# Kernel tuning notes

Measured on AMD Instinct MI355X. Metric: run time of the kernel, lower is better.

Reference implementation:

```python
import jax, jax.numpy as jnp
import numpy as np

N, E = 50000, 800000
IN_DIM, E_DIM, OUT_DIM, H = 128, 32, 16, 4
NEG_SLOPE = 0.2


def setup_inputs() -> dict:
    key = jax.random.key(0)
    ks = jax.random.split(key, 9)
    return {
        "feat": jax.random.normal(ks[0], (N, IN_DIM), jnp.float32),
        "edge_attr": jax.random.normal(ks[1], (E, E_DIM), jnp.float32),
        "src": jax.random.randint(ks[2], (E,), 0, N),
        "dst": jax.random.randint(ks[3], (E,), 0, N),
        "W_fc": jax.random.normal(ks[4], (OUT_DIM * H, IN_DIM), jnp.float32) * 0.1,
        "W_edge": jax.random.normal(ks[5], (OUT_DIM * H, E_DIM), jnp.float32) * 0.1,
        "attn_h": jax.random.normal(ks[6], (1, H, OUT_DIM), jnp.float32) * 0.1,
        "attn_t": jax.random.normal(ks[7], (1, H, OUT_DIM), jnp.float32) * 0.1,
        "attn_e": jax.random.normal(ks[8], (1, H, OUT_DIM), jnp.float32) * 0.1,
        "bias": jnp.zeros((1, H, OUT_DIM), jnp.float32),
    }


def reference(feat, edge_attr, src, dst, W_fc, W_edge, attn_h, attn_t, attn_e, bias):
    n = feat.shape[0]
    # node / edge projections
    feat_ = (feat @ W_fc.T).reshape(n, H, OUT_DIM)          # [N,H,D]
    eh = (feat_ * attn_h).sum(-1)                            # [N,H]
    et = (feat_ * attn_t).sum(-1)                            # [N,H]
    feat_e = (edge_attr @ W_edge.T).reshape(-1, H, OUT_DIM)  # [E,H,D]
    ee = (feat_e * attn_e).sum(-1)                           # [E,H]
    # per-edge attention logits: u_add_e then e_add_v, then leaky relu
    e = eh[src] + ee + et[dst]                               # [E,H]
    e = jnp.where(e > 0, e, NEG_SLOPE * e)
    # edge softmax grouped by destination node
    e_max = jax.ops.segment_max(e, dst, num_segments=n)      # [N,H]
    e_max = jnp.where(jnp.isfinite(e_max), e_max, 0.0)
    a = jnp.exp(e - e_max[dst])                              # [E,H]
    a_sum = jax.ops.segment_sum(a, dst, num_segments=n)      # [N,H]
    a = a / jnp.where(a_sum[dst] > 0, a_sum[dst], 1.0)
    # u_mul_e + sum aggregation
    msg = feat_[src] * a[:, :, None]                         # [E,H,D]
    rst = jax.ops.segment_sum(msg, dst, num_segments=n)      # [N,H,D]
    rst = rst + bias
    return rst.reshape(n, H * OUT_DIM)                       # concat_out
```

## Files before the change

kernel.cpp:

```cpp
#include <hip/hip_runtime.h>

#define NN 50000
#define EE 800000
#define IND 128
#define EDD 32
#define ODD 16
#define NH 4
#define HD 64
#define NEG_SLOPE 0.2f
#define NBLK ((NN + 255) / 256)

__global__ __launch_bounds__(256)
void k_init(int* __restrict__ deg) {
    int i = blockIdx.x * 256 + threadIdx.x;
    if (i < NN) deg[i] = 0;
}

__global__ __launch_bounds__(256)
void k_prep(const float* __restrict__ W_fc, const float* __restrict__ W_edge,
            const float* __restrict__ attn_e,
            float* __restrict__ Wt, float* __restrict__ w_ee) {
    int i = blockIdx.x * 256 + threadIdx.x;
    if (i < HD * IND) {
        int k = i >> 6, j = i & 63;
        Wt[i] = W_fc[j * IND + k];
    }
    if (i < NH * EDD) {
        int h = i >> 5, k = i & 31;
        float s = 0.f;
        for (int d = 0; d < ODD; ++d)
            s += W_edge[(h * ODD + d) * EDD + k] * attn_e[h * ODD + d];
        w_ee[i] = s;
    }
}

__global__ __launch_bounds__(256)
void k_node(const float* __restrict__ feat, const float* __restrict__ Wt,
            const float* __restrict__ attn_h, const float* __restrict__ attn_t,
            float* __restrict__ feat_ws, float2* __restrict__ eh2,
            float2* __restrict__ et2) {
    int n = blockIdx.x * 256 + threadIdx.x;
    int half = blockIdx.y;
    if (n >= NN) return;
    const int jbase = half * 32;
    float4 row[32];
    const float4* fr4 = (const float4*)(feat + (long)n * IND);
#pragma unroll
    for (int q = 0; q < 32; ++q) row[q] = fr4[q];
    float acc[32];
#pragma unroll
    for (int j = 0; j < 32; ++j) acc[j] = 0.f;
#pragma unroll 4
    for (int k0 = 0; k0 < 32; ++k0) {
        float f[4] = {row[k0].x, row[k0].y, row[k0].z, row[k0].w};
#pragma unroll
        for (int kk = 0; kk < 4; ++kk) {
            const float* w = Wt + (k0 * 4 + kk) * HD + jbase;
#pragma unroll
            for (int j = 0; j < 32; ++j) acc[j] += f[kk] * w[j];
        }
    }
    float4* d4 = (float4*)(feat_ws + (long)n * HD + jbase);
#pragma unroll
    for (int q = 0; q < 8; ++q)
        d4[q] = make_float4(acc[q*4], acc[q*4+1], acc[q*4+2], acc[q*4+3]);
    float sh[2], st[2];
#pragma unroll
    for (int hh = 0; hh < 2; ++hh) {
        sh[hh] = 0.f; st[hh] = 0.f;
        int hg = half * 2 + hh;
#pragma unroll
        for (int d = 0; d < ODD; ++d) {
            float av = acc[hh * ODD + d];
            sh[hh] += av * attn_h[hg * ODD + d];
            st[hh] += av * attn_t[hg * ODD + d];
        }
    }
    eh2[n * 2 + half] = make_float2(sh[0], sh[1]);
    et2[n * 2 + half] = make_float2(st[0], st[1]);
}

__global__ __launch_bounds__(256)
void k_hist(const int* __restrict__ dst, int* __restrict__ deg, int* __restrict__ rank) {
    int e = blockIdx.x * 256 + threadIdx.x;
    if (e < EE) rank[e] = atomicAdd(&deg[dst[e]], 1);
}

__global__ __launch_bounds__(256)
void k_scan1(const int* __restrict__ deg, int* __restrict__ offs, int* __restrict__ part) {
    __shared__ int s[256];
    int t = threadIdx.x, i = blockIdx.x * 256 + t;
    int v = (i < NN) ? deg[i] : 0;
    s[t] = v;
    __syncthreads();
#pragma unroll
    for (int o = 1; o < 256; o <<= 1) {
        int u = (t >= o) ? s[t - o] : 0;
        __syncthreads();
        if (t >= o) s[t] += u;
        __syncthreads();
    }
    if (i < NN) offs[i] = s[t] - v;
    if (t == 255) part[blockIdx.x] = s[255];
}

__global__ __launch_bounds__(256)
void k_scan2(int* __restrict__ part) {
    __shared__ int s[256];
    int t = threadIdx.x;
    int v = (t < NBLK) ? part[t] : 0;
    s[t] = v;
    __syncthreads();
#pragma unroll
    for (int o = 1; o < 256; o <<= 1) {
        int u = (t >= o) ? s[t - o] : 0;
        __syncthreads();
        if (t >= o) s[t] += u;
        __syncthreads();
    }
    if (t < NBLK) part[t] = s[t] - v;
}

__global__ __launch_bounds__(256)
void k_scan3(int* __restrict__ offs, const int* __restrict__ part) {
    int i = blockIdx.x * 256 + threadIdx.x;
    if (i < NN) offs[i] += part[i >> 8];
}

__global__ __launch_bounds__(256)
void k_logit(const float* __restrict__ edge_attr, const int* __restrict__ src,
             const int* __restrict__ dst, const float* __restrict__ w_ee,
             const float4* __restrict__ eh4, const float4* __restrict__ et4,
             const int* __restrict__ offs, const int* __restrict__ rank,
             float4* __restrict__ e_buf4, int* __restrict__ perm) {
    int e = blockIdx.x * 256 + threadIdx.x;
    if (e >= EE) return;
    int s_ = src[e], d_ = dst[e];
    int pos = offs[d_] + rank[e];
    float4 vh = eh4[s_];
    float4 vt = et4[d_];
    const float* ea = edge_attr + (long)e * EDD;
    float f[EDD];
#pragma unroll
    for (int c = 0; c < 8; ++c) {
        float4 p = *(const float4*)(ea + c * 4);
        f[c*4+0] = p.x; f[c*4+1] = p.y; f[c*4+2] = p.z; f[c*4+3] = p.w;
    }
    float x[NH];
#pragma unroll
    for (int h = 0; h < NH; ++h) {
        float s = 0.f;
#pragma unroll
        for (int k = 0; k < EDD; ++k) s += f[k] * w_ee[h * EDD + k];
        x[h] = s;
    }
    x[0] += vh.x + vt.x; x[1] += vh.y + vt.y;
    x[2] += vh.z + vt.z; x[3] += vh.w + vt.w;
#pragma unroll
    for (int h = 0; h < NH; ++h) {
        float v = x[h];
        v = v > 0.f ? v : NEG_SLOPE * v;
        x[h] = __expf(v);
    }
    e_buf4[e] = make_float4(x[0], x[1], x[2], x[3]);
    perm[pos] = e;
}

__global__ __launch_bounds__(256)
void k_reduce(const int* __restrict__ offs, const int* __restrict__ deg,
              const float* __restrict__ e_buf, const int* __restrict__ perm,
              const int* __restrict__ src, const float* __restrict__ feat_ws,
              const float* __restrict__ bias, float* __restrict__ out) {
    int wid = (blockIdx.x * 256 + threadIdx.x) >> 6;
    int lane = threadIdx.x & 63;
    if (wid >= NN) return;
    int start = __builtin_amdgcn_readfirstlane(offs[wid]);
    int dn    = __builtin_amdgcn_readfirstlane(deg[wid]);
    int h = lane >> 4;
    int q = lane & 15;
    float acc = 0.f, l = 0.f;

    for (int c0 = 0; c0 < dn; c0 += 16) {
        int rem = dn - c0; if (rem > 16) rem = 16;
        int qq = (q < rem) ? q : (rem - 1);
        int   e_q = perm[start + c0 + qq];
        int   s_q = src[e_q];
        float a_q = (q < rem) ? e_buf[(long)e_q * 4 + h] : 0.f;
        float f[16];
#pragma unroll
        for (int i = 0; i < 16; ++i) {
            int si = __shfl(s_q, i);
            f[i] = feat_ws[(long)si * HD + lane];
        }
#pragma unroll
        for (int i = 0; i < 16; ++i) {
            float ai = __shfl(a_q, (lane & 48) + i);
            l += ai;
            acc += ai * f[i];
        }
    }
    float res = (l > 0.f) ? acc / l : 0.f;
    out[(long)wid * HD + lane] = res + bias[lane];
}

extern "C" void kernel_launch(void* const* d_in, const int* in_sizes, int n_in,
                              void* d_out, int out_size, void* d_ws, size_t ws_size,
                              hipStream_t stream) {
    const float* feat      = (const float*)d_in[0];
    const float* edge_attr = (const float*)d_in[1];
    const int*   src       = (const int*)d_in[2];
    const int*   dst       = (const int*)d_in[3];
    const float* W_fc      = (const float*)d_in[4];
    const float* W_edge    = (const float*)d_in[5];
    const float* attn_h    = (const float*)d_in[6];
    const float* attn_t    = (const float*)d_in[7];
    const float* attn_e    = (const float*)d_in[8];
    const float* bias      = (const float*)d_in[9];
    float* out             = (float*)d_out;

    float* ws        = (float*)d_ws;
    float4* e_buf4   = (float4*)ws;
    float4* eh4      = e_buf4 + EE;
    float4* et4      = eh4 + NN;
    float*  feat_ws  = (float*)(et4 + NN);
    float*  Wt       = feat_ws + (long)NN * HD;
    float*  w_ee     = Wt + HD * IND;
    int*    perm     = (int*)(w_ee + NH * EDD);
    int*    rank     = perm + EE;
    int*    deg      = rank + EE;
    int*    offs     = deg + NN;
    int*    part     = offs + NN;

    k_init<<<NBLK, 256, 0, stream>>>(deg);
    k_prep<<<(HD * IND + 255) / 256, 256, 0, stream>>>(W_fc, W_edge, attn_e, Wt, w_ee);
    dim3 ngrid(NBLK, 2);
    k_node<<<ngrid, 256, 0, stream>>>(feat, Wt, attn_h, attn_t, feat_ws,
                                      (float2*)eh4, (float2*)et4);
    k_hist<<<(EE + 255) / 256, 256, 0, stream>>>(dst, deg, rank);
    k_scan1<<<NBLK, 256, 0, stream>>>(deg, offs, part);
    k_scan2<<<1, 256, 0, stream>>>(part);
    k_scan3<<<NBLK, 256, 0, stream>>>(offs, part);
    k_logit<<<(EE + 255) / 256, 256, 0, stream>>>(edge_attr, src, dst, w_ee, eh4, et4,
                                                  offs, rank, e_buf4, perm);
    k_reduce<<<(NN * 64 + 255) / 256, 256, 0, stream>>>(offs, deg, (const float*)e_buf4,
                                                        perm, src, feat_ws, bias, out);
}
```

Measured before the change: 350.1 us.

## Store node features as bf16 and write attention in dst-sorted order for reduce

Projected node features are packed to bf16, which halves the bytes gathered per edge in the reduce kernel. The logit kernel is split into a permutation scatter and an attention kernel that runs in sorted (dst) order, writing attention weights and source ids contiguously. The reduce kernel can then read them with coalesced loads instead of double indirection through perm. The init and prep kernels are fused and the node loop is fully unrolled. The cost is bf16 rounding error on the features, an extra launch, and random edge_attr reads in k_att.

```diff
diff --git a/kernel.cpp b/kernel.cpp
--- a/kernel.cpp
+++ b/kernel.cpp
@@ -10,17 +10,21 @@
 #define NEG_SLOPE 0.2f
 #define NBLK ((NN + 255) / 256)
 
-__global__ __launch_bounds__(256)
-void k_init(int* __restrict__ deg) {
+typedef unsigned int u32;
+typedef unsigned short u16;
+
+__device__ __forceinline__ float bf2f(u32 u) { return __uint_as_float(u << 16); }
+__device__ __forceinline__ u16 f2bf(float f) {
+    u32 b = __float_as_uint(f);
+    return (u16)((b + 0x7FFF + ((b >> 16) & 1)) >> 16);
+}
+
+__global__ __launch_bounds__(256)
+void k_init_prep(int* __restrict__ deg, const float* __restrict__ W_fc,
+                 const float* __restrict__ W_edge, const float* __restrict__ attn_e,
+                 float* __restrict__ Wt, float* __restrict__ w_ee) {
     int i = blockIdx.x * 256 + threadIdx.x;
     if (i < NN) deg[i] = 0;
-}
-
-__global__ __launch_bounds__(256)
-void k_prep(const float* __restrict__ W_fc, const float* __restrict__ W_edge,
-            const float* __restrict__ attn_e,
-            float* __restrict__ Wt, float* __restrict__ w_ee) {
-    int i = blockIdx.x * 256 + threadIdx.x;
     if (i < HD * IND) {
         int k = i >> 6, j = i & 63;
         Wt[i] = W_fc[j * IND + k];
@@ -37,7 +41,7 @@
 __global__ __launch_bounds__(256)
 void k_node(const float* __restrict__ feat, const float* __restrict__ Wt,
             const float* __restrict__ attn_h, const float* __restrict__ attn_t,
-            float* __restrict__ feat_ws, float2* __restrict__ eh2,
+            u16* __restrict__ feat_bf, float2* __restrict__ eh2,
             float2* __restrict__ et2) {
     int n = blockIdx.x * 256 + threadIdx.x;
     int half = blockIdx.y;
@@ -47,10 +51,11 @@
     const float4* fr4 = (const float4*)(feat + (long)n * IND);
 #pragma unroll
     for (int q = 0; q < 32; ++q) row[q] = fr4[q];
+    asm volatile("" ::: "memory");
     float acc[32];
 #pragma unroll
     for (int j = 0; j < 32; ++j) acc[j] = 0.f;
-#pragma unroll 4
+#pragma unroll
     for (int k0 = 0; k0 < 32; ++k0) {
         float f[4] = {row[k0].x, row[k0].y, row[k0].z, row[k0].w};
 #pragma unroll
@@ -60,10 +65,14 @@
             for (int j = 0; j < 32; ++j) acc[j] += f[kk] * w[j];
         }
     }
-    float4* d4 = (float4*)(feat_ws + (long)n * HD + jbase);
-#pragma unroll
-    for (int q = 0; q < 8; ++q)
-        d4[q] = make_float4(acc[q*4], acc[q*4+1], acc[q*4+2], acc[q*4+3]);
+    u32 pk[16];
+#pragma unroll
+    for (int q = 0; q < 16; ++q)
+        pk[q] = (u32)f2bf(acc[q * 2]) | ((u32)f2bf(acc[q * 2 + 1]) << 16);
+    uint4* d4 = (uint4*)((u32*)(feat_bf + (long)n * HD + jbase));
+#pragma unroll
+    for (int q = 0; q < 4; ++q)
+        d4[q] = make_uint4(pk[q*4], pk[q*4+1], pk[q*4+2], pk[q*4+3]);
     float sh[2], st[2];
 #pragma unroll
     for (int hh = 0; hh < 2; ++hh) {
@@ -128,24 +137,30 @@
 }
 
 __global__ __launch_bounds__(256)
-void k_logit(const float* __restrict__ edge_attr, const int* __restrict__ src,
-             const int* __restrict__ dst, const float* __restrict__ w_ee,
-             const float4* __restrict__ eh4, const float4* __restrict__ et4,
-             const int* __restrict__ offs, const int* __restrict__ rank,
-             float4* __restrict__ e_buf4, int* __restrict__ perm) {
+void k_perm(const int* __restrict__ dst, const int* __restrict__ rank,
+            const int* __restrict__ offs, int* __restrict__ perm) {
     int e = blockIdx.x * 256 + threadIdx.x;
-    if (e >= EE) return;
+    if (e < EE) perm[offs[dst[e]] + rank[e]] = e;
+}
+
+__global__ __launch_bounds__(256)
+void k_att(const float* __restrict__ edge_attr, const int* __restrict__ src,
+           const int* __restrict__ dst, const float* __restrict__ w_ee,
+           const float4* __restrict__ eh4, const float4* __restrict__ et4,
+           const int* __restrict__ perm, float4* __restrict__ a4,
+           int* __restrict__ ssrc) {
+    int pos = blockIdx.x * 256 + threadIdx.x;
+    if (pos >= EE) return;
+    int e = perm[pos];
     int s_ = src[e], d_ = dst[e];
-    int pos = offs[d_] + rank[e];
     float4 vh = eh4[s_];
     float4 vt = et4[d_];
-    const float* ea = edge_attr + (long)e * EDD;
-    float f[EDD];
-#pragma unroll
-    for (int c = 0; c < 8; ++c) {
-        float4 p = *(const float4*)(ea + c * 4);
-        f[c*4+0] = p.x; f[c*4+1] = p.y; f[c*4+2] = p.z; f[c*4+3] = p.w;
-    }
+    const float4* ea = (const float4*)(edge_attr + (long)e * EDD);
+    float4 r[8];
+#pragma unroll
+    for (int c = 0; c < 8; ++c) r[c] = ea[c];
+    asm volatile("" ::: "memory");
+    const float* f = (const float*)r;
     float x[NH];
 #pragma unroll
     for (int h = 0; h < NH; ++h) {
@@ -162,15 +177,15 @@
         v = v > 0.f ? v : NEG_SLOPE * v;
         x[h] = __expf(v);
     }
-    e_buf4[e] = make_float4(x[0], x[1], x[2], x[3]);
-    perm[pos] = e;
+    a4[pos] = make_float4(x[0], x[1], x[2], x[3]);
+    ssrc[pos] = s_;
 }
 
 __global__ __launch_bounds__(256)
 void k_reduce(const int* __restrict__ offs, const int* __restrict__ deg,
-              const float* __restrict__ e_buf, const int* __restrict__ perm,
-              const int* __restrict__ src, const float* __restrict__ feat_ws,
-              const float* __restrict__ bias, float* __restrict__ out) {
+              const float* __restrict__ a_flat, const int* __restrict__ ssrc,
+              const u16* __restrict__ feat_bf, const float* __restrict__ bias,
+              float* __restrict__ out) {
     int wid = (blockIdx.x * 256 + threadIdx.x) >> 6;
     int lane = threadIdx.x & 63;
     if (wid >= NN) return;
@@ -182,21 +197,22 @@
 
     for (int c0 = 0; c0 < dn; c0 += 16) {
         int rem = dn - c0; if (rem > 16) rem = 16;
+        float av = (lane < rem * 4) ? a_flat[(start + c0) * 4 + lane] : 0.f;
+        float a_q = __shfl(av, 4 * (lane & 15) + (lane >> 4));
+        if (q >= rem) a_q = 0.f;
         int qq = (q < rem) ? q : (rem - 1);
-        int   e_q = perm[start + c0 + qq];
-        int   s_q = src[e_q];
-        float a_q = (q < rem) ? e_buf[(long)e_q * 4 + h] : 0.f;
-        float f[16];
+        int s_q = ssrc[start + c0 + qq];
+        u32 uf[16];
 #pragma unroll
         for (int i = 0; i < 16; ++i) {
             int si = __shfl(s_q, i);
-            f[i] = feat_ws[(long)si * HD + lane];
+            uf[i] = feat_bf[(long)si * HD + lane];
         }
 #pragma unroll
         for (int i = 0; i < 16; ++i) {
             float ai = __shfl(a_q, (lane & 48) + i);
             l += ai;
-            acc += ai * f[i];
+            acc += ai * bf2f(uf[i]);
         }
     }
     float res = (l > 0.f) ? acc / l : 0.f;
@@ -218,30 +234,31 @@
     const float* bias      = (const float*)d_in[9];
     float* out             = (float*)d_out;
 
-    float* ws        = (float*)d_ws;
-    float4* e_buf4   = (float4*)ws;
-    float4* eh4      = e_buf4 + EE;
-    float4* et4      = eh4 + NN;
-    float*  feat_ws  = (float*)(et4 + NN);
-    float*  Wt       = feat_ws + (long)NN * HD;
-    float*  w_ee     = Wt + HD * IND;
-    int*    perm     = (int*)(w_ee + NH * EDD);
-    int*    rank     = perm + EE;
-    int*    deg      = rank + EE;
-    int*    offs     = deg + NN;
-    int*    part     = offs + NN;
-
-    k_init<<<NBLK, 256, 0, stream>>>(deg);
-    k_prep<<<(HD * IND + 255) / 256, 256, 0, stream>>>(W_fc, W_edge, attn_e, Wt, w_ee);
+    float* ws       = (float*)d_ws;
+    float4* a4      = (float4*)ws;
+    float4* eh4     = a4 + EE;
+    float4* et4     = eh4 + NN;
+    u16*   feat_bf  = (u16*)(et4 + NN);
+    float* Wt       = (float*)(feat_bf + (long)NN * HD);
+    float* w_ee     = Wt + HD * IND;
+    int*   perm     = (int*)(w_ee + NH * EDD);
+    int*   rank     = perm + EE;
+    int*   ssrc     = rank + EE;
+    int*   deg      = ssrc + EE;
+    int*   offs     = deg + NN;
+    int*   part     = offs + NN;
+
+    k_init_prep<<<NBLK, 256, 0, stream>>>(deg, W_fc, W_edge, attn_e, Wt, w_ee);
     dim3 ngrid(NBLK, 2);
-    k_node<<<ngrid, 256, 0, stream>>>(feat, Wt, attn_h, attn_t, feat_ws,
+    k_node<<<ngrid, 256, 0, stream>>>(feat, Wt, attn_h, attn_t, feat_bf,
                                       (float2*)eh4, (float2*)et4);
     k_hist<<<(EE + 255) / 256, 256, 0, stream>>>(dst, deg, rank);
     k_scan1<<<NBLK, 256, 0, stream>>>(deg, offs, part);
     k_scan2<<<1, 256, 0, stream>>>(part);
     k_scan3<<<NBLK, 256, 0, stream>>>(offs, part);
-    k_logit<<<(EE + 255) / 256, 256, 0, stream>>>(edge_attr, src, dst, w_ee, eh4, et4,
-                                                  offs, rank, e_buf4, perm);
-    k_reduce<<<(NN * 64 + 255) / 256, 256, 0, stream>>>(offs, deg, (const float*)e_buf4,
-                                                        perm, src, feat_ws, bias, out);
-}
+    k_perm<<<(EE + 255) / 256, 256, 0, stream>>>(dst, rank, offs, perm);
+    k_att<<<(EE + 255) / 256, 256, 0, stream>>>(edge_attr, src, dst, w_ee, eh4, et4,
+                                                perm, a4, ssrc);
+    k_reduce<<<(NN * 64 + 255) / 256, 256, 0, stream>>>(offs, deg, (const float*)a4,
+                                                        ssrc, feat_bf, bias, out);
+}
```

After: 563.4 us. +60.9%, slower.
